# Optimization experiments

Hardware: AMD Instinct MI355X
Metric: run time of the kernel (lower is better)

## Reference

```python
import jax, jax.numpy as jnp
import numpy as np

B, S, HID = 2, 2048, 2048
HQ, HKV, D = 32, 4, 128
EPS = 1e-6
SCALE = D ** -0.5


def _rms_norm(x, w):
    # per-head RMSNorm over last dim, computed in fp32 like the torch module
    xf = x.astype(jnp.float32)
    var = jnp.mean(xf * xf, axis=-1, keepdims=True)
    return (w * (xf * jax.lax.rsqrt(var + EPS))).astype(x.dtype)


def _rotate_half(x):
    x1, x2 = jnp.split(x, 2, axis=-1)
    return jnp.concatenate([-x2, x1], axis=-1)


def setup_inputs() -> dict:
    key = jax.random.key(0)
    ks = jax.random.split(key, 8)
    hidden_states = jax.random.normal(ks[0], (B, S, HID), dtype=jnp.float32)
    # RoPE tables (HF Qwen style, theta=1e6)
    inv_freq = 1.0 / (1e6 ** (np.arange(0, D, 2, dtype=np.float32) / D))
    t = np.arange(S, dtype=np.float32)
    freqs = np.outer(t, inv_freq)                      # [S, D/2]
    emb = np.concatenate([freqs, freqs], axis=-1)      # [S, D]
    cos = jnp.asarray(np.cos(emb))
    sin = jnp.asarray(np.sin(emb))
    sd = HID ** -0.5
    wq = jax.random.normal(ks[1], (HID, HQ * D), dtype=jnp.float32) * sd
    wk = jax.random.normal(ks[2], (HID, HKV * D), dtype=jnp.float32) * sd
    wv = jax.random.normal(ks[3], (HID, HKV * D), dtype=jnp.float32) * sd
    wo = jax.random.normal(ks[4], (HQ * D, HID), dtype=jnp.float32) * ((HQ * D) ** -0.5)
    q_norm_w = jnp.ones((D,), dtype=jnp.float32)
    k_norm_w = jnp.ones((D,), dtype=jnp.float32)
    return {"hidden_states": hidden_states, "cos": cos, "sin": sin,
            "wq": wq, "wk": wk, "wv": wv, "wo": wo,
            "q_norm_w": q_norm_w, "k_norm_w": k_norm_w}


def reference(hidden_states, cos, sin, wq, wk, wv, wo, q_norm_w, k_norm_w):
    b, s, _ = hidden_states.shape
    # QKV projection (no bias)
    q = (hidden_states @ wq).reshape(b, s, HQ, D)
    k = (hidden_states @ wk).reshape(b, s, HKV, D)
    v = (hidden_states @ wv).reshape(b, s, HKV, D)
    # per-head RMSNorm on q, k
    q = _rms_norm(q, q_norm_w)
    k = _rms_norm(k, k_norm_w)
    # RoPE: cos/sin [s, D] -> broadcast over batch and heads
    c = cos[None, :, None, :]
    sn = sin[None, :, None, :]
    q = q * c + _rotate_half(q) * sn
    k = k * c + _rotate_half(k) * sn
    # [b, h, s, d]
    q = q.transpose(0, 2, 1, 3)
    k = k.transpose(0, 2, 1, 3)
    v = v.transpose(0, 2, 1, 3)
    # GQA: repeat kv heads to match query heads
    groups = HQ // HKV
    k = jnp.repeat(k, groups, axis=1)
    v = jnp.repeat(v, groups, axis=1)
    # causal SDPA (prefill)
    scores = jnp.einsum('bhqd,bhkd->bhqk', q, k) * SCALE
    causal = jnp.tril(jnp.ones((s, s), dtype=bool))
    scores = jnp.where(causal[None, None], scores, jnp.finfo(scores.dtype).min)
    attn = jax.nn.softmax(scores, axis=-1)
    out = jnp.einsum('bhqk,bhkd->bhqd', attn, v)
    out = out.transpose(0, 2, 1, 3).reshape(b, s, HQ * D)
    return out @ wo
```

## Files before the change

kernel.cpp:

```cpp
#include <hip/hip_runtime.h>
#include <hip/hip_bf16.h>
#include <stdint.h>

typedef __bf16 bf16;
typedef __bf16 bf16x4 __attribute__((ext_vector_type(4)));
typedef __bf16 bf16x8 __attribute__((ext_vector_type(8)));
typedef float floatx4 __attribute__((ext_vector_type(4)));

#define MFMA16(a, b, c) __builtin_amdgcn_mfma_f32_16x16x32_bf16((a), (b), (c), 0, 0, 0)

static __device__ __forceinline__ void async_load16(const bf16* g, bf16* l) {
    __builtin_amdgcn_global_load_lds(
        (const __attribute__((address_space(1))) uint32_t*)(const void*)g,
        (__attribute__((address_space(3))) uint32_t*)(void*)l,
        16, 0, 0);
}

static __device__ __forceinline__ bf16x8 load8(const bf16* p) {
    return *(const bf16x8*)p;
}
static __device__ __forceinline__ bf16x8 load8(const float* p) {
    const float4 a = *(const float4*)p;
    const float4 b = *(const float4*)(p + 4);
    bf16x8 r;
    r[0] = (bf16)a.x; r[1] = (bf16)a.y; r[2] = (bf16)a.z; r[3] = (bf16)a.w;
    r[4] = (bf16)b.x; r[5] = (bf16)b.y; r[6] = (bf16)b.z; r[7] = (bf16)b.w;
    return r;
}

__global__ __launch_bounds__(256) void f2b(const float* __restrict__ in,
                                           bf16* __restrict__ out) {
    const size_t i = ((size_t)blockIdx.x * 256 + threadIdx.x) * 8;
    *(bf16x8*)&out[i] = load8(in + i);
}

__global__ __launch_bounds__(256) void transposeF2B(const float* __restrict__ in,
                                                    bf16* __restrict__ out,
                                                    int R, int C) {
    __shared__ float t[32][33];
    const int c0 = blockIdx.x * 32, r0 = blockIdx.y * 32;
    const int tx = threadIdx.x & 31, ty = threadIdx.x >> 5;
#pragma unroll
    for (int i = 0; i < 4; i++)
        t[ty + i * 8][tx] = in[(size_t)(r0 + ty + i * 8) * C + c0 + tx];
    __syncthreads();
#pragma unroll
    for (int i = 0; i < 4; i++)
        out[(size_t)(c0 + ty + i * 8) * R + r0 + tx] = (bf16)t[tx][ty + i * 8];
}

__global__ __launch_bounds__(256) void gemm_qkv(const bf16* __restrict__ A,
                                                const bf16* __restrict__ BT,
                                                bf16* __restrict__ Q,
                                                bf16* __restrict__ K2,
                                                bf16* __restrict__ Vt) {
    constexpr int K = 2048;
    __shared__ __attribute__((aligned(16))) bf16 As[128 * 32];
    __shared__ __attribute__((aligned(16))) bf16 Bs[128 * 32];
    const int tid = threadIdx.x;
    const int wave = tid >> 6, lane = tid & 63;
    const int quad = lane >> 4, l16 = lane & 15;
    const int m0 = blockIdx.y * 128, n0 = blockIdx.x * 128;
    const int wr = (wave >> 1) * 64, wc = (wave & 1) * 64;

    floatx4 acc[4][4] = {};

    const bf16* gA = A + (size_t)(m0 + wave * 32 + (lane >> 2)) * K + (lane & 3) * 8;
    const bf16* gB = BT + (size_t)(n0 + wave * 32 + (lane >> 2)) * K + (lane & 3) * 8;

    for (int k0 = 0; k0 < K; k0 += 32) {
        async_load16(gA + k0, &As[(wave * 32) * 32]);
        async_load16(gA + k0 + 16 * (size_t)K, &As[(wave * 32 + 16) * 32]);
        async_load16(gB + k0, &Bs[(wave * 32) * 32]);
        async_load16(gB + k0 + 16 * (size_t)K, &Bs[(wave * 32 + 16) * 32]);
        __syncthreads();

        bf16x8 af[4], bfr[4];
#pragma unroll
        for (int i = 0; i < 4; i++)
            af[i] = *(const bf16x8*)&As[(wr + i * 16 + l16) * 32 + quad * 8];
#pragma unroll
        for (int j = 0; j < 4; j++)
            bfr[j] = *(const bf16x8*)&Bs[(wc + j * 16 + l16) * 32 + quad * 8];
#pragma unroll
        for (int i = 0; i < 4; i++)
#pragma unroll
            for (int j = 0; j < 4; j++)
                acc[i][j] = MFMA16(af[i], bfr[j], acc[i][j]);
        __syncthreads();
    }

    const int region = (n0 >= 4608) ? 2 : (n0 >= 4096 ? 1 : 0);
#pragma unroll
    for (int i = 0; i < 4; i++) {
#pragma unroll
        for (int j = 0; j < 4; j++) {
            const int row = m0 + wr + i * 16 + quad * 4;
            const int col = n0 + wc + j * 16 + l16;
            if (region == 0) {
#pragma unroll
                for (int r = 0; r < 4; r++)
                    Q[(size_t)(row + r) * 4096 + col] = (bf16)acc[i][j][r];
            } else if (region == 1) {
#pragma unroll
                for (int r = 0; r < 4; r++)
                    K2[(size_t)(row + r) * 512 + (col - 4096)] = (bf16)acc[i][j][r];
            } else {
                bf16x4 t;
#pragma unroll
                for (int r = 0; r < 4; r++) t[r] = (bf16)acc[i][j][r];
                *(bf16x4*)&Vt[(size_t)(col - 4608) * 4096 + row] = t;
            }
        }
    }
}

__global__ __launch_bounds__(256) void gemm_o(const bf16* __restrict__ A,
                                              const bf16* __restrict__ BT,
                                              float* __restrict__ C) {
    constexpr int K = 4096, N = 2048;
    __shared__ __attribute__((aligned(16))) bf16 As[128 * 32];
    __shared__ __attribute__((aligned(16))) bf16 Bs[128 * 32];
    const int tid = threadIdx.x;
    const int wave = tid >> 6, lane = tid & 63;
    const int quad = lane >> 4, l16 = lane & 15;
    const int m0 = blockIdx.y * 128, n0 = blockIdx.x * 128;
    const int wr = (wave >> 1) * 64, wc = (wave & 1) * 64;

    floatx4 acc[4][4] = {};

    const bf16* gA = A + (size_t)(m0 + wave * 32 + (lane >> 2)) * K + (lane & 3) * 8;
    const bf16* gB = BT + (size_t)(n0 + wave * 32 + (lane >> 2)) * K + (lane & 3) * 8;

    for (int k0 = 0; k0 < K; k0 += 32) {
        async_load16(gA + k0, &As[(wave * 32) * 32]);
        async_load16(gA + k0 + 16 * (size_t)K, &As[(wave * 32 + 16) * 32]);
        async_load16(gB + k0, &Bs[(wave * 32) * 32]);
        async_load16(gB + k0 + 16 * (size_t)K, &Bs[(wave * 32 + 16) * 32]);
        __syncthreads();

        bf16x8 af[4], bfr[4];
#pragma unroll
        for (int i = 0; i < 4; i++)
            af[i] = *(const bf16x8*)&As[(wr + i * 16 + l16) * 32 + quad * 8];
#pragma unroll
        for (int j = 0; j < 4; j++)
            bfr[j] = *(const bf16x8*)&Bs[(wc + j * 16 + l16) * 32 + quad * 8];
#pragma unroll
        for (int i = 0; i < 4; i++)
#pragma unroll
            for (int j = 0; j < 4; j++)
                acc[i][j] = MFMA16(af[i], bfr[j], acc[i][j]);
        __syncthreads();
    }

#pragma unroll
    for (int i = 0; i < 4; i++) {
#pragma unroll
        for (int j = 0; j < 4; j++) {
            const int row = m0 + wr + i * 16 + quad * 4;
            const int col = n0 + wc + j * 16 + l16;
#pragma unroll
            for (int r = 0; r < 4; r++)
                C[(size_t)(row + r) * N + col] = acc[i][j][r];
        }
    }
}

__global__ __launch_bounds__(256) void rmsrope(bf16* __restrict__ x,
                                               const float* __restrict__ w,
                                               const float* __restrict__ cosb,
                                               const float* __restrict__ sinb,
                                               int nh, int S) {
    const int lane = threadIdx.x & 63;
    const int row = blockIdx.x * 4 + (threadIdx.x >> 6);
    const int s = (row / nh) % S;
    bf16* p = x + (size_t)row * 128;
    float x1 = (float)p[lane];
    float x2 = (float)p[lane + 64];
    float ssq = x1 * x1 + x2 * x2;
#pragma unroll
    for (int m = 1; m < 64; m <<= 1) ssq += __shfl_xor(ssq, m);
    const float r = rsqrtf(ssq * (1.0f / 128.0f) + 1e-6f);
    const float y1 = w[lane] * x1 * r;
    const float y2 = w[lane + 64] * x2 * r;
    const float c1 = cosb[s * 128 + lane];
    const float s1 = sinb[s * 128 + lane];
    const float c2 = cosb[s * 128 + lane + 64];
    const float s2 = sinb[s * 128 + lane + 64];
    p[lane] = (bf16)(y1 * c1 - y2 * s1);
    p[lane + 64] = (bf16)(y2 * c2 + y1 * s2);
}

__global__ __launch_bounds__(256) void attn(bf16* QO,
                                            const bf16* __restrict__ Km,
                                            const bf16* __restrict__ Vt,
                                            int S) {
    __shared__ __attribute__((aligned(16))) bf16 Kl[64 * 128];
    __shared__ __attribute__((aligned(16))) bf16 Vl[128 * 64];
    __shared__ __attribute__((aligned(16))) bf16 Pl[4][16 * 40];

    const int tid = threadIdx.x, wave = tid >> 6, lane = tid & 63;
    const int quad = lane >> 4, l16 = lane & 15;
    const int h = blockIdx.y, b = blockIdx.z;
    const int kvh = h >> 3;
    const float scale = 0.08838834764831845f;

    const bf16* Kg = Km + (size_t)b * S * 512 + kvh * 128;
    const bf16* Vg = Vt + (size_t)kvh * 128 * 4096 + (size_t)b * S;

    const bf16* kSrc[4]; bf16* kDst[4];
    const bf16* vSrc[4]; bf16* vDst[4];
#pragma unroll
    for (int j = 0; j < 4; j++) {
        const int krow = wave * 16 + 4 * j + (lane >> 4);
        kSrc[j] = Kg + (size_t)krow * 512 + (((lane & 15) ^ (krow & 7)) << 3);
        kDst[j] = &Kl[(wave * 16 + 4 * j) * 128];
        const int vrow = wave * 32 + 8 * j + (lane >> 3);
        vSrc[j] = Vg + (size_t)vrow * 4096 + (((lane & 7) ^ (vrow & 7)) << 3);
        vDst[j] = &Vl[(wave * 32 + 8 * j) * 64];
    }

    bf16* pw = &Pl[wave][0];
    const int NT = S / 64;

#pragma unroll
    for (int half = 0; half < 2; half++) {
        const int qt = half ? (NT - 1 - blockIdx.x) : blockIdx.x;
        const int qb = qt * 64 + wave * 16;

        bf16x8 qf[4];
        {
            const bf16* qrow = QO + (size_t)(b * S + qb + l16) * 4096 + h * 128 + quad * 8;
#pragma unroll
            for (int c = 0; c < 4; c++) qf[c] = *(const bf16x8*)(qrow + c * 32);
        }

        floatx4 o_acc[8] = {};
        float l_i[4] = {0.f, 0.f, 0.f, 0.f};

        const int kend = qt * 64 + 64;
        for (int k0 = 0; k0 < kend; k0 += 64) {
#pragma unroll
            for (int j = 0; j < 4; j++)
                async_load16(kSrc[j] + (size_t)k0 * 512, kDst[j]);
#pragma unroll
            for (int j = 0; j < 4; j++)
                async_load16(vSrc[j] + k0, vDst[j]);
            __syncthreads();

            floatx4 sc[4] = {};
#pragma unroll
            for (int c = 0; c < 4; c++) {
                const int slot = ((c * 4 + quad) ^ (l16 & 7)) << 3;
#pragma unroll
                for (int m = 0; m < 4; m++) {
                    const bf16x8 kf = *(const bf16x8*)&Kl[(l16 + 16 * m) * 128 + slot];
                    sc[m] = MFMA16(qf[c], kf, sc[m]);
                }
            }

#pragma unroll
            for (int ks = 0; ks < 2; ks++) {
                const int kb = k0 + ks * 32;
                if (kb > qb + 15) continue;
                const floatx4 s0 = sc[2 * ks], s1 = sc[2 * ks + 1];
                if (kb + 31 > qb) {
#pragma unroll
                    for (int r = 0; r < 4; r++) {
                        const int qi = qb + quad * 4 + r;
                        const float p0 = (kb + l16 > qi) ? 0.f : __expf(s0[r] * scale);
                        const float p1 = (kb + 16 + l16 > qi) ? 0.f : __expf(s1[r] * scale);
                        l_i[r] += p0 + p1;
                        pw[(quad * 4 + r) * 40 + l16] = (bf16)p0;
                        pw[(quad * 4 + r) * 40 + l16 + 16] = (bf16)p1;
                    }
                } else {
#pragma unroll
                    for (int r = 0; r < 4; r++) {
                        const float p0 = __expf(s0[r] * scale);
                        const float p1 = __expf(s1[r] * scale);
                        l_i[r] += p0 + p1;
                        pw[(quad * 4 + r) * 40 + l16] = (bf16)p0;
                        pw[(quad * 4 + r) * 40 + l16 + 16] = (bf16)p1;
                    }
                }
                const bf16x8 pa = *(const bf16x8*)&pw[l16 * 40 + quad * 8];
#pragma unroll
                for (int c = 0; c < 8; c++) {
                    const int vps = ((ks * 4 + quad) ^ (l16 & 7)) << 3;
                    const bf16x8 vf = *(const bf16x8*)&Vl[(c * 16 + l16) * 64 + vps];
                    o_acc[c] = MFMA16(pa, vf, o_acc[c]);
                }
            }
            __syncthreads();
        }

#pragma unroll
        for (int r = 0; r < 4; r++) {
            float l = l_i[r];
            l += __shfl_xor(l, 1);
            l += __shfl_xor(l, 2);
            l += __shfl_xor(l, 4);
            l += __shfl_xor(l, 8);
            const float inv = (l > 0.f) ? 1.0f / l : 0.f;
            const size_t orow = (size_t)(b * S + qb + quad * 4 + r) * 4096 + h * 128;
#pragma unroll
            for (int c = 0; c < 8; c++)
                QO[orow + c * 16 + l16] = (bf16)(o_acc[c][r] * inv);
        }
    }
}

template <typename TA, typename TB, typename TC>
__global__ __launch_bounds__(256) void gemm_bn(const TA* __restrict__ A,
                                               const TB* __restrict__ B,
                                               TC* __restrict__ C,
                                               int M, int N, int K) {
    __shared__ __attribute__((aligned(16))) bf16 As[128 * 32];
    __shared__ __attribute__((aligned(16))) bf16 Bs[128 * 32];
    const int tid = threadIdx.x;
    const int wave = tid >> 6, lane = tid & 63;
    const int quad = lane >> 4, l16 = lane & 15;
    const int m0 = blockIdx.y * 128, n0 = blockIdx.x * 128;
    const int wr = (wave >> 1) * 64, wc = (wave & 1) * 64;
    floatx4 acc[4][4] = {};
    const int r0 = tid >> 2;
    const int kc = (tid & 3) * 8;
    const TA* gA0 = A + (size_t)(m0 + r0) * K + kc;
    const TA* gA1 = A + (size_t)(m0 + 64 + r0) * K + kc;
    const int kr = tid & 31;
    const int nc8 = (tid >> 5) * 8;
    const TB* gB = B + (size_t)kr * N + n0 + nc8;
    for (int k0 = 0; k0 < K; k0 += 32) {
        const bf16x8 a0 = load8(gA0 + k0);
        const bf16x8 a1 = load8(gA1 + k0);
        const TB* gBk = gB + (size_t)k0 * N;
        const bf16x8 b0 = load8(gBk);
        const bf16x8 b1 = load8(gBk + 64);
        __syncthreads();
        *(bf16x8*)&As[r0 * 32 + kc] = a0;
        *(bf16x8*)&As[(64 + r0) * 32 + kc] = a1;
#pragma unroll
        for (int j = 0; j < 8; j++) {
            Bs[(nc8 + j) * 32 + kr] = b0[j];
            Bs[(nc8 + 64 + j) * 32 + kr] = b1[j];
        }
        __syncthreads();
        bf16x8 af[4], bfr[4];
#pragma unroll
        for (int i = 0; i < 4; i++)
            af[i] = *(const bf16x8*)&As[(wr + i * 16 + l16) * 32 + quad * 8];
#pragma unroll
        for (int j = 0; j < 4; j++)
            bfr[j] = *(const bf16x8*)&Bs[(wc + j * 16 + l16) * 32 + quad * 8];
#pragma unroll
        for (int i = 0; i < 4; i++)
#pragma unroll
            for (int j = 0; j < 4; j++)
                acc[i][j] = MFMA16(af[i], bfr[j], acc[i][j]);
    }
#pragma unroll
    for (int i = 0; i < 4; i++) {
#pragma unroll
        for (int j = 0; j < 4; j++) {
            const int row = m0 + wr + i * 16 + quad * 4;
            const int col = n0 + wc + j * 16 + l16;
#pragma unroll
            for (int r = 0; r < 4; r++)
                C[(size_t)(row + r) * N + col] = (TC)acc[i][j][r];
        }
    }
}

__global__ __launch_bounds__(256) void attn_fb(bf16* QO,
                                               const bf16* __restrict__ Km,
                                               const bf16* __restrict__ Vm,
                                               int S) {
    __shared__ __attribute__((aligned(16))) bf16 Kl[32 * 136];
    __shared__ __attribute__((aligned(16))) bf16 Vl[128 * 40];
    __shared__ __attribute__((aligned(16))) bf16 Pl[4][16 * 40];
    const int tid = threadIdx.x, wave = tid >> 6, lane = tid & 63;
    const int quad = lane >> 4, l16 = lane & 15;
    const int q0 = blockIdx.x * 64;
    const int h = blockIdx.y, b = blockIdx.z;
    const int kvh = h >> 3;
    const int q_base = q0 + wave * 16;
    const float scale = 0.08838834764831845f;
    bf16x8 qf[4];
    {
        const bf16* qrow = QO + (size_t)(b * S + q_base + l16) * 4096 + h * 128 + quad * 8;
#pragma unroll
        for (int c = 0; c < 4; c++) qf[c] = *(const bf16x8*)(qrow + c * 32);
    }
    floatx4 o_acc[8] = {};
    float l_i[4] = {0.f, 0.f, 0.f, 0.f};
    const int kend = q0 + 64;
    for (int k0 = 0; k0 < kend; k0 += 32) {
#pragma unroll
        for (int it = 0; it < 2; ++it) {
            const int cc = tid + it * 256;
            const int row = cc >> 4;
            const int off = (cc & 15) * 8;
            const size_t gidx = (size_t)(b * S + k0 + row) * 512 + kvh * 128 + off;
            const bf16x8 kv = *(const bf16x8*)&Km[gidx];
            const bf16x8 vv = *(const bf16x8*)&Vm[gidx];
            *(bf16x8*)&Kl[row * 136 + off] = kv;
#pragma unroll
            for (int j = 0; j < 8; j++) Vl[(off + j) * 40 + row] = vv[j];
        }
        __syncthreads();
        if (k0 <= q_base + 15) {
            floatx4 sc0 = {}, sc1 = {};
#pragma unroll
            for (int c = 0; c < 4; c++) {
                bf16x8 b0 = *(const bf16x8*)&Kl[l16 * 136 + c * 32 + quad * 8];
                bf16x8 b1 = *(const bf16x8*)&Kl[(l16 + 16) * 136 + c * 32 + quad * 8];
                sc0 = MFMA16(qf[c], b0, sc0);
                sc1 = MFMA16(qf[c], b1, sc1);
            }
            const bool edge = (k0 + 31 > q_base);
            bf16* pw = &Pl[wave][0];
#pragma unroll
            for (int r = 0; r < 4; r++) {
                const int qi = q_base + quad * 4 + r;
                const bool mk0 = edge && (k0 + l16 > qi);
                const bool mk1 = edge && (k0 + 16 + l16 > qi);
                const float p0 = mk0 ? 0.f : __expf(sc0[r] * scale);
                const float p1 = mk1 ? 0.f : __expf(sc1[r] * scale);
                l_i[r] += p0 + p1;
                pw[(quad * 4 + r) * 40 + l16] = (bf16)p0;
                pw[(quad * 4 + r) * 40 + l16 + 16] = (bf16)p1;
            }
            const bf16x8 pa = *(const bf16x8*)&pw[l16 * 40 + quad * 8];
#pragma unroll
            for (int c = 0; c < 8; c++) {
                const bf16x8 vf = *(const bf16x8*)&Vl[(c * 16 + l16) * 40 + quad * 8];
                o_acc[c] = MFMA16(pa, vf, o_acc[c]);
            }
        }
        __syncthreads();
    }
#pragma unroll
    for (int r = 0; r < 4; r++) {
        float l = l_i[r];
        l += __shfl_xor(l, 1);
        l += __shfl_xor(l, 2);
        l += __shfl_xor(l, 4);
        l += __shfl_xor(l, 8);
        const float inv = (l > 0.f) ? 1.0f / l : 0.f;
        const size_t orow = (size_t)(b * S + q_base + quad * 4 + r) * 4096 + h * 128;
#pragma unroll
        for (int c = 0; c < 8; c++)
            QO[orow + c * 16 + l16] = (bf16)(o_acc[c][r] * inv);
    }
}

extern "C" void kernel_launch(void* const* d_in, const int* in_sizes, int n_in,
                              void* d_out, int out_size, void* d_ws, size_t ws_size,
                              hipStream_t stream) {
    const float* hidden = (const float*)d_in[0];
    const float* cosb = (const float*)d_in[1];
    const float* sinb = (const float*)d_in[2];
    const float* wq = (const float*)d_in[3];
    const float* wk = (const float*)d_in[4];
    const float* wv = (const float*)d_in[5];
    const float* wo = (const float*)d_in[6];
    const float* qnw = (const float*)d_in[7];
    const float* knw = (const float*)d_in[8];
    float* out = (float*)d_out;

    constexpr int B = 2, S = 2048, HID = 2048, HQ = 32, HKV = 4, D = 128;
    constexpr int M = B * S;
    constexpr int NQ = HQ * D;
    constexpr int NKV = HKV * D;
    constexpr int NQKV = NQ + 2 * NKV;

    const size_t need = ((size_t)NQKV * HID + (size_t)HID * NQ +
                         (size_t)M * NQ + 2 * (size_t)M * NKV) * sizeof(bf16);

    if (ws_size >= need) {
        bf16* p = (bf16*)d_ws;
        bf16* wqkvT = p; p += (size_t)NQKV * HID;
        bf16* X = p;     p += (size_t)HID * NQ;
        bf16* Qb = p;    p += (size_t)M * NQ;
        bf16* Kb = p;    p += (size_t)M * NKV;
        bf16* Vt = p;    p += (size_t)NKV * M;

        transposeF2B<<<dim3(NQ / 32, HID / 32), 256, 0, stream>>>(wq, wqkvT, HID, NQ);
        transposeF2B<<<dim3(NKV / 32, HID / 32), 256, 0, stream>>>(wk, wqkvT + (size_t)NQ * HID, HID, NKV);
        transposeF2B<<<dim3(NKV / 32, HID / 32), 256, 0, stream>>>(wv, wqkvT + (size_t)(NQ + NKV) * HID, HID, NKV);

        f2b<<<dim3((M * HID) / (256 * 8)), 256, 0, stream>>>(hidden, X);

        gemm_qkv<<<dim3(NQKV / 128, M / 128), 256, 0, stream>>>(X, wqkvT, Qb, Kb, Vt);

        rmsrope<<<dim3(M * HQ / 4), 256, 0, stream>>>(Qb, qnw, cosb, sinb, HQ, S);
        rmsrope<<<dim3(M * HKV / 4), 256, 0, stream>>>(Kb, knw, cosb, sinb, HKV, S);

        attn<<<dim3(S / 128, HQ, B), 256, 0, stream>>>(Qb, Kb, Vt, S);

        transposeF2B<<<dim3(HID / 32, NQ / 32), 256, 0, stream>>>(wo, X, NQ, HID);
        gemm_o<<<dim3(HID / 128, M / 128), 256, 0, stream>>>(Qb, X, out);
    } else {
        bf16* p = (bf16*)d_ws;
        bf16* Qb = p;  p += (size_t)M * NQ;
        bf16* Kb = p;  p += (size_t)M * NKV;
        bf16* Vb = p;  p += (size_t)M * NKV;

        gemm_bn<float, float, bf16><<<dim3(NQ / 128, M / 128), 256, 0, stream>>>(hidden, wq, Qb, M, NQ, HID);
        gemm_bn<float, float, bf16><<<dim3(NKV / 128, M / 128), 256, 0, stream>>>(hidden, wk, Kb, M, NKV, HID);
        gemm_bn<float, float, bf16><<<dim3(NKV / 128, M / 128), 256, 0, stream>>>(hidden, wv, Vb, M, NKV, HID);
        rmsrope<<<dim3(M * HQ / 4), 256, 0, stream>>>(Qb, qnw, cosb, sinb, HQ, S);
        rmsrope<<<dim3(M * HKV / 4), 256, 0, stream>>>(Kb, knw, cosb, sinb, HKV, S);
        attn_fb<<<dim3(S / 64, HQ, B), 256, 0, stream>>>(Qb, Kb, Vb, S);
        gemm_bn<bf16, float, float><<<dim3(HID / 128, M / 128), 256, 0, stream>>>(Qb, wo, out, M, HID, NQ);
    }
}
```

Baseline: 519.8 us.

## Double-buffer K/V tiles and widen attention blocks to eight waves

The attention kernel now runs 512 threads per block, each covering 128 query rows, and double-buffers the K/V tiles in LDS. The next tile is prefetched asynchronously while the current one is computed, using explicit vmcnt waits and barriers. Waves whose rows lie entirely before a tile skip its compute. This aims to hide global load latency and halve K/V reloads per query, at the cost of more LDS and fewer blocks. The hardcoded 15 assumes S=2048.

```diff
diff --git a/kernel.cpp b/kernel.cpp
--- a/kernel.cpp
+++ b/kernel.cpp
@@ -192,13 +192,13 @@
     p[lane + 64] = (bf16)(y2 * c2 + y1 * s2);
 }
 
-__global__ __launch_bounds__(256) void attn(bf16* QO,
-                                            const bf16* __restrict__ Km,
-                                            const bf16* __restrict__ Vt,
-                                            int S) {
-    __shared__ __attribute__((aligned(16))) bf16 Kl[64 * 128];
-    __shared__ __attribute__((aligned(16))) bf16 Vl[128 * 64];
-    __shared__ __attribute__((aligned(16))) bf16 Pl[4][16 * 40];
+__global__ __launch_bounds__(512, 4) void attn(bf16* QO,
+                                               const bf16* __restrict__ Km,
+                                               const bf16* __restrict__ Vt,
+                                               int S) {
+    __shared__ __attribute__((aligned(16))) bf16 Kl[2][64 * 128];
+    __shared__ __attribute__((aligned(16))) bf16 Vl[2][128 * 64];
+    __shared__ __attribute__((aligned(16))) bf16 Pl[8][16 * 40];
 
     const int tid = threadIdx.x, wave = tid >> 6, lane = tid & 63;
     const int quad = lane >> 4, l16 = lane & 15;
@@ -209,25 +209,31 @@
     const bf16* Kg = Km + (size_t)b * S * 512 + kvh * 128;
     const bf16* Vg = Vt + (size_t)kvh * 128 * 4096 + (size_t)b * S;
 
-    const bf16* kSrc[4]; bf16* kDst[4];
-    const bf16* vSrc[4]; bf16* vDst[4];
-#pragma unroll
-    for (int j = 0; j < 4; j++) {
-        const int krow = wave * 16 + 4 * j + (lane >> 4);
-        kSrc[j] = Kg + (size_t)krow * 512 + (((lane & 15) ^ (krow & 7)) << 3);
-        kDst[j] = &Kl[(wave * 16 + 4 * j) * 128];
-        const int vrow = wave * 32 + 8 * j + (lane >> 3);
-        vSrc[j] = Vg + (size_t)vrow * 4096 + (((lane & 7) ^ (vrow & 7)) << 3);
-        vDst[j] = &Vl[(wave * 32 + 8 * j) * 64];
-    }
+    const int krow0 = wave * 8 + (lane >> 4);
+    const int krow1 = wave * 8 + 4 + (lane >> 4);
+    const bf16* kSrc0 = Kg + (size_t)krow0 * 512 + (((lane & 15) ^ (krow0 & 7)) << 3);
+    const bf16* kSrc1 = Kg + (size_t)krow1 * 512 + (((lane & 15) ^ (krow1 & 7)) << 3);
+    const int vrow0 = wave * 16 + (lane >> 3);
+    const int vrow1 = wave * 16 + 8 + (lane >> 3);
+    const bf16* vSrc0 = Vg + (size_t)vrow0 * 4096 + (((lane & 7) ^ (vrow0 & 7)) << 3);
+    const bf16* vSrc1 = Vg + (size_t)vrow1 * 4096 + (((lane & 7) ^ (vrow1 & 7)) << 3);
+
+#define STAGE(buf, kk)                                                  \
+    do {                                                                \
+        bf16* kb_ = &Kl[buf][(wave * 8) * 128];                         \
+        bf16* vb_ = &Vl[buf][(wave * 16) * 64];                         \
+        async_load16(kSrc0 + (size_t)(kk) * 512, kb_);                  \
+        async_load16(kSrc1 + (size_t)(kk) * 512, kb_ + 4 * 128);        \
+        async_load16(vSrc0 + (kk), vb_);                                \
+        async_load16(vSrc1 + (kk), vb_ + 8 * 64);                       \
+    } while (0)
 
     bf16* pw = &Pl[wave][0];
-    const int NT = S / 64;
 
 #pragma unroll
     for (int half = 0; half < 2; half++) {
-        const int qt = half ? (NT - 1 - blockIdx.x) : blockIdx.x;
-        const int qb = qt * 64 + wave * 16;
+        const int qt = half ? (15 - blockIdx.x) : blockIdx.x;
+        const int qb = qt * 128 + wave * 16;
 
         bf16x8 qf[4];
         {
@@ -239,61 +245,71 @@
         floatx4 o_acc[8] = {};
         float l_i[4] = {0.f, 0.f, 0.f, 0.f};
 
-        const int kend = qt * 64 + 64;
-        for (int k0 = 0; k0 < kend; k0 += 64) {
-#pragma unroll
-            for (int j = 0; j < 4; j++)
-                async_load16(kSrc[j] + (size_t)k0 * 512, kDst[j]);
-#pragma unroll
-            for (int j = 0; j < 4; j++)
-                async_load16(vSrc[j] + k0, vDst[j]);
-            __syncthreads();
-
-            floatx4 sc[4] = {};
-#pragma unroll
-            for (int c = 0; c < 4; c++) {
-                const int slot = ((c * 4 + quad) ^ (l16 & 7)) << 3;
-#pragma unroll
-                for (int m = 0; m < 4; m++) {
-                    const bf16x8 kf = *(const bf16x8*)&Kl[(l16 + 16 * m) * 128 + slot];
-                    sc[m] = MFMA16(qf[c], kf, sc[m]);
+        const int nt = 2 * (qt + 1);
+        STAGE(0, 0);
+
+        for (int kt = 0; kt < nt; ++kt) {
+            const int k0 = kt * 64;
+            const int cur = kt & 1;
+            if (kt + 1 < nt) {
+                STAGE(cur ^ 1, (kt + 1) * 64);
+                asm volatile("s_waitcnt vmcnt(4)" ::: "memory");
+            } else {
+                asm volatile("s_waitcnt vmcnt(0)" ::: "memory");
+            }
+            __builtin_amdgcn_s_barrier();
+            __builtin_amdgcn_sched_barrier(0);
+
+            if (k0 <= qb + 15) {
+                const bf16* kl = &Kl[cur][0];
+                const bf16* vl = &Vl[cur][0];
+
+                floatx4 sc[4] = {};
+#pragma unroll
+                for (int c = 0; c < 4; c++) {
+                    const int slot = ((c * 4 + quad) ^ (l16 & 7)) << 3;
+#pragma unroll
+                    for (int m = 0; m < 4; m++) {
+                        const bf16x8 kf = *(const bf16x8*)&kl[(l16 + 16 * m) * 128 + slot];
+                        sc[m] = MFMA16(qf[c], kf, sc[m]);
+                    }
+                }
+
+#pragma unroll
+                for (int ks = 0; ks < 2; ks++) {
+                    const int kb = k0 + ks * 32;
+                    if (kb > qb + 15) continue;
+                    const floatx4 s0 = sc[2 * ks], s1 = sc[2 * ks + 1];
+                    if (kb + 31 > qb) {
+#pragma unroll
+                        for (int r = 0; r < 4; r++) {
+                            const int qi = qb + quad * 4 + r;
+                            const float p0 = (kb + l16 > qi) ? 0.f : __expf(s0[r] * scale);
+                            const float p1 = (kb + 16 + l16 > qi) ? 0.f : __expf(s1[r] * scale);
+                            l_i[r] += p0 + p1;
+                            pw[(quad * 4 + r) * 40 + l16] = (bf16)p0;
+                            pw[(quad * 4 + r) * 40 + l16 + 16] = (bf16)p1;
+                        }
+                    } else {
+#pragma unroll
+                        for (int r = 0; r < 4; r++) {
+                            const float p0 = __expf(s0[r] * scale);
+                            const float p1 = __expf(s1[r] * scale);
+                            l_i[r] += p0 + p1;
+                            pw[(quad * 4 + r) * 40 + l16] = (bf16)p0;
+                            pw[(quad * 4 + r) * 40 + l16 + 16] = (bf16)p1;
+                        }
+                    }
+                    const bf16x8 pa = *(const bf16x8*)&pw[l16 * 40 + quad * 8];
+#pragma unroll
+                    for (int c = 0; c < 8; c++) {
+                        const int vps = ((ks * 4 + quad) ^ (l16 & 7)) << 3;
+                        const bf16x8 vf = *(const bf16x8*)&vl[(c * 16 + l16) * 64 + vps];
+                        o_acc[c] = MFMA16(pa, vf, o_acc[c]);
+                    }
                 }
             }
-
-#pragma unroll
-            for (int ks = 0; ks < 2; ks++) {
-                const int kb = k0 + ks * 32;
-                if (kb > qb + 15) continue;
-                const floatx4 s0 = sc[2 * ks], s1 = sc[2 * ks + 1];
-                if (kb + 31 > qb) {
-#pragma unroll
-                    for (int r = 0; r < 4; r++) {
-                        const int qi = qb + quad * 4 + r;
-                        const float p0 = (kb + l16 > qi) ? 0.f : __expf(s0[r] * scale);
-                        const float p1 = (kb + 16 + l16 > qi) ? 0.f : __expf(s1[r] * scale);
-                        l_i[r] += p0 + p1;
-                        pw[(quad * 4 + r) * 40 + l16] = (bf16)p0;
-                        pw[(quad * 4 + r) * 40 + l16 + 16] = (bf16)p1;
-                    }
-                } else {
-#pragma unroll
-                    for (int r = 0; r < 4; r++) {
-                        const float p0 = __expf(s0[r] * scale);
-                        const float p1 = __expf(s1[r] * scale);
-                        l_i[r] += p0 + p1;
-                        pw[(quad * 4 + r) * 40 + l16] = (bf16)p0;
-                        pw[(quad * 4 + r) * 40 + l16 + 16] = (bf16)p1;
-                    }
-                }
-                const bf16x8 pa = *(const bf16x8*)&pw[l16 * 40 + quad * 8];
-#pragma unroll
-                for (int c = 0; c < 8; c++) {
-                    const int vps = ((ks * 4 + quad) ^ (l16 & 7)) << 3;
-                    const bf16x8 vf = *(const bf16x8*)&Vl[(c * 16 + l16) * 64 + vps];
-                    o_acc[c] = MFMA16(pa, vf, o_acc[c]);
-                }
-            }
-            __syncthreads();
+            __builtin_amdgcn_s_barrier();
         }
 
 #pragma unroll
@@ -310,6 +326,7 @@
                 QO[orow + c * 16 + l16] = (bf16)(o_acc[c][r] * inv);
         }
     }
+#undef STAGE
 }
 
 template <typename TA, typename TB, typename TC>
@@ -498,7 +515,7 @@
         rmsrope<<<dim3(M * HQ / 4), 256, 0, stream>>>(Qb, qnw, cosb, sinb, HQ, S);
         rmsrope<<<dim3(M * HKV / 4), 256, 0, stream>>>(Kb, knw, cosb, sinb, HKV, S);
 
-        attn<<<dim3(S / 128, HQ, B), 256, 0, stream>>>(Qb, Kb, Vt, S);
+        attn<<<dim3(S / 256, HQ, B), 512, 0, stream>>>(Qb, Kb, Vt, S);
 
         transposeF2B<<<dim3(HID / 32, NQ / 32), 256, 0, stream>>>(wo, X, NQ, HID);
         gemm_o<<<dim3(HID / 128, M / 128), 256, 0, stream>>>(Qb, X, out);
```

Result: faster. 500.1 us (-3.8%).
